# Kernel tuning notes

Measured on AMD Instinct MI355X. Metric: run time of the kernel, lower is better.

Reference implementation:

```python
import jax, jax.numpy as jnp
import numpy as np
from jax import lax

B, T, F_, CIN, COUT, NAUX = 32, 1000, 80, 1, 64, 128
KH, KW = 3, 3            # cnn_ker
CPAD = (1, 1)            # floor(k/2)
CSTR = (1, 1)
PK, PSTR = (2, 2), (2, 2)  # max-pool kernel/stride, pad 0


def setup_inputs() -> dict:
    key = jax.random.key(0)
    k1, k2, k3, k4, k5, k6, k7 = jax.random.split(key, 7)
    x = jax.random.normal(k1, (B, T, F_), dtype=jnp.float32)
    x_len = jax.random.randint(k2, (B,), 0, 1000).astype(jnp.int32)
    aux = jax.random.normal(k3, (B, NAUX), dtype=jnp.float32)
    # hypernetwork (filter/bias generator) params
    Wg = jax.random.normal(k4, (CIN * COUT * KH * KW, NAUX), dtype=jnp.float32) * 0.05
    bg = jax.random.normal(k5, (CIN * COUT * KH * KW,), dtype=jnp.float32) * 0.05
    Wb = jax.random.normal(k6, (COUT, NAUX), dtype=jnp.float32) * 0.05
    bb = jax.random.normal(k7, (COUT,), dtype=jnp.float32) * 0.05
    return {"x": x, "x_len": x_len, "aux": aux, "Wg": Wg, "bg": bg, "Wb": Wb, "bb": bb}


def _calclen(L, p, d, k, s):
    return (L + 2 * p - d * (k - 1) - 1) // s + 1


def reference(x, x_len, aux, Wg, bg, Wb, bb):
    # hypernetwork: per-sample conv filters [B, COUT, CIN, KH, KW] and biases [B, COUT]
    filt = (aux @ Wg.T + bg).reshape(B, COUT, CIN, KH, KW)
    bias = aux @ Wb.T + bb
    # per-sample conv as a single grouped conv: groups = B
    xg = x.reshape(1, B * CIN, T, F_)                 # x is [B, T, F] with CIN=1
    fg = filt.reshape(B * COUT, CIN, KH, KW)
    y = lax.conv_general_dilated(
        xg, fg, window_strides=CSTR,
        padding=[(CPAD[0], CPAD[0]), (CPAD[1], CPAD[1])],
        dimension_numbers=("NCHW", "OIHW", "NCHW"),
        feature_group_count=B)
    y = y.reshape(B, COUT, T, F_) + bias[:, :, None, None]
    # activ = relu
    y = jax.nn.relu(y)
    # max pool (2,2), stride (2,2), no pad
    y = lax.reduce_window(y, -jnp.inf, lax.max,
                          (1, 1, PK[0], PK[1]), (1, 1, PSTR[0], PSTR[1]), "VALID")
    # length propagation + time masking
    l1 = _calclen(x_len, CPAD[0], 1, KH, CSTR[0])
    l2 = _calclen(l1, 0, 1, PK[0], PSTR[0])
    t_out = y.shape[2]
    mask = jnp.arange(t_out)[None, :] >= l2[:, None]          # [B, T_out]
    y = jnp.where(mask[:, None, :, None], jnp.float32(0.0), y)
    return y, l2
```

## Files before the change

### kernel.cpp

```cpp
#include <hip/hip_runtime.h>
#include <hip/hip_fp16.h>
#include <stdint.h>

#define B_    32
#define T_    1000
#define F_    80
#define COUT_ 64
#define NAUX_ 128
#define TO_   500
#define FO_   40
#define PSTR_ 12
#define CL_   8

typedef float v4f __attribute__((ext_vector_type(4)));
typedef _Float16 h2v __attribute__((ext_vector_type(2)));
typedef __fp16 fp16x2 __attribute__((ext_vector_type(2)));

__global__ __launch_bounds__(256) void hyper_kernel(
    const float* __restrict__ aux,
    const float* __restrict__ Wg,
    const float* __restrict__ bg,
    const float* __restrict__ Wb,
    const float* __restrict__ bb,
    const int*   __restrict__ x_len,
    uint32_t* __restrict__ fw,
    float* __restrict__ l2_out)
{
    const int NFT = B_ * 576 * 16;
    const int NBT = B_ * 64 * 16;
    int t = blockIdx.x * blockDim.x + threadIdx.x;

    if (t < NFT) {
        int d = t >> 4, part = t & 15;
        int b = d / 576, idx = d % 576;
        const float* a = aux + b * NAUX_ + part * 8;
        const float* w = Wg + (size_t)idx * NAUX_ + part * 8;
        float4 a0 = *(const float4*)(a);
        float4 a1 = *(const float4*)(a + 4);
        float4 w0 = *(const float4*)(w);
        float4 w1 = *(const float4*)(w + 4);
        float s = a0.x * w0.x;
        s = fmaf(a0.y, w0.y, s);
        s = fmaf(a0.z, w0.z, s);
        s = fmaf(a0.w, w0.w, s);
        s = fmaf(a1.x, w1.x, s);
        s = fmaf(a1.y, w1.y, s);
        s = fmaf(a1.z, w1.z, s);
        s = fmaf(a1.w, w1.w, s);
        s += __shfl_xor(s, 1);
        s += __shfl_xor(s, 2);
        s += __shfl_xor(s, 4);
        s += __shfl_xor(s, 8);
        if (part == 0) {
            int c = idx / 9, k = idx % 9;
            uint32_t hu = (uint32_t)__half_as_ushort(__float2half_rn(s + bg[idx]));
            fw[(b * COUT_ + c) * PSTR_ + k] = hu | (hu << 16);
        }
    } else if (t < NFT + NBT) {
        int u = t - NFT;
        int d = u >> 4, part = u & 15;
        int b = d >> 6, c = d & 63;
        const float* a = aux + b * NAUX_ + part * 8;
        const float* w = Wb + (size_t)c * NAUX_ + part * 8;
        float4 a0 = *(const float4*)(a);
        float4 a1 = *(const float4*)(a + 4);
        float4 w0 = *(const float4*)(w);
        float4 w1 = *(const float4*)(w + 4);
        float s = a0.x * w0.x;
        s = fmaf(a0.y, w0.y, s);
        s = fmaf(a0.z, w0.z, s);
        s = fmaf(a0.w, w0.w, s);
        s = fmaf(a1.x, w1.x, s);
        s = fmaf(a1.y, w1.y, s);
        s = fmaf(a1.z, w1.z, s);
        s = fmaf(a1.w, w1.w, s);
        s += __shfl_xor(s, 1);
        s += __shfl_xor(s, 2);
        s += __shfl_xor(s, 4);
        s += __shfl_xor(s, 8);
        if (part == 0) fw[d * PSTR_ + 9] = __float_as_uint(s + bb[c]);
    } else if (t < NFT + NBT + B_) {
        int b = t - NFT - NBT;
        l2_out[b] = (float)(x_len[b] >> 1);
    }
}

__global__ __launch_bounds__(256) void conv_pool_kernel(
    const float*    __restrict__ x,
    const int*      __restrict__ x_len,
    const uint32_t* __restrict__ fw,
    float* __restrict__ out)
{
    const int bg  = blockIdx.y;
    const int b   = bg >> 3;
    const int bc0 = bg * CL_;

    int t = blockIdx.x * blockDim.x + threadIdx.x;
    if (t >= TO_ * 10) return;
    int f4 = t % 10;
    int to = t / 10;

    float* obase = out + ((size_t)bc0 * TO_ + to) * FO_ + 4 * f4;

    int l2 = x_len[b] >> 1;
    if (to >= l2) {
        v4f z = (v4f){0.f, 0.f, 0.f, 0.f};
        #pragma unroll
        for (int i = 0; i < CL_; ++i)
            __builtin_nontemporal_store(z, (v4f*)(obase + (size_t)i * (TO_ * FO_)));
        return;
    }

    const uint32_t* p = fw + (size_t)bc0 * PSTR_;
    uint32_t prm[CL_][10];
    #pragma unroll
    for (int i = 0; i < CL_; ++i)
        #pragma unroll
        for (int k = 0; k < 10; ++k)
            prm[i][k] = p[i * PSTR_ + k];

    float w[4][10];
    const float* xb = x + (size_t)b * (T_ * F_);
    const int cbase = 8 * f4;
    #pragma unroll
    for (int i = 0; i < 4; ++i) {
        int r = 2 * to - 1 + i;
        if (r < 0 || r >= T_) {
            #pragma unroll
            for (int j = 0; j < 10; ++j) w[i][j] = 0.f;
        } else {
            const float* rp = xb + r * F_ + cbase;
            w[i][0] = (f4 > 0) ? rp[-1] : 0.f;
            float4 m0 = *(const float4*)(rp);
            float4 m1 = *(const float4*)(rp + 4);
            w[i][1] = m0.x; w[i][2] = m0.y; w[i][3] = m0.z; w[i][4] = m0.w;
            w[i][5] = m1.x; w[i][6] = m1.y; w[i][7] = m1.z; w[i][8] = m1.w;
            w[i][9] = (f4 < 9) ? rp[8] : 0.f;
        }
    }

    __half2 wp[3][10];
    #pragma unroll
    for (int ii = 0; ii < 3; ++ii)
        #pragma unroll
        for (int c = 0; c < 10; ++c) {
            fp16x2 pk = __builtin_amdgcn_cvt_pkrtz(w[ii][c], w[ii + 1][c]);
            wp[ii][c] = *(__half2*)&pk;
        }

    #pragma unroll
    for (int i = 0; i < CL_; ++i) {
        __half2 flt[9];
        #pragma unroll
        for (int k = 0; k < 9; ++k)
            flt[k] = *(const __half2*)&prm[i][k];
        const float bias = __uint_as_float(prm[i][9]);

        float o[4];
        #pragma unroll
        for (int q = 0; q < 4; ++q) {
            __half2 acc0 = __halves2half2(__ushort_as_half((unsigned short)0),
                                          __ushort_as_half((unsigned short)0));
            __half2 acc1 = acc0;
            #pragma unroll
            for (int ii = 0; ii < 3; ++ii) {
                #pragma unroll
                for (int jj = 0; jj < 3; ++jj) {
                    const __half2 f = flt[ii * 3 + jj];
                    acc0 = __hfma2(f, wp[ii][2 * q + jj],     acc0);
                    acc1 = __hfma2(f, wp[ii][2 * q + 1 + jj], acc1);
                }
            }
            h2v m2 = __builtin_elementwise_max(*(h2v*)&acc0, *(h2v*)&acc1);
            float m = fmaxf((float)m2.x, (float)m2.y);
            o[q] = fmaxf(m + bias, 0.f);
        }
        v4f ov = (v4f){o[0], o[1], o[2], o[3]};
        __builtin_nontemporal_store(ov, (v4f*)(obase + (size_t)i * (TO_ * FO_)));
    }
}

extern "C" void kernel_launch(void* const* d_in, const int* in_sizes, int n_in,
                              void* d_out, int out_size, void* d_ws, size_t ws_size,
                              hipStream_t stream) {
    const float* x     = (const float*)d_in[0];
    const int*   x_len = (const int*)d_in[1];
    const float* aux   = (const float*)d_in[2];
    const float* Wg    = (const float*)d_in[3];
    const float* bg    = (const float*)d_in[4];
    const float* Wb    = (const float*)d_in[5];
    const float* bb    = (const float*)d_in[6];

    float*    out = (float*)d_out;
    uint32_t* fw  = (uint32_t*)d_ws;
    float* l2_out = out + (size_t)B_ * COUT_ * TO_ * FO_;

    {
        int total = B_ * 576 * 16 + B_ * 64 * 16 + B_;
        int blocks = (total + 255) / 256;
        hipLaunchKernelGGL(hyper_kernel, dim3(blocks), dim3(256), 0, stream,
                           aux, Wg, bg, Wb, bb, x_len, fw, l2_out);
    }
    {
        hipLaunchKernelGGL(conv_pool_kernel, dim3(20, 256), dim3(256), 0, stream,
                           x, x_len, fw, out);
    }
}
```

Before: 43.63 us.

## Pre-pack input row pairs to fp16x2 in workspace before conv-pool

The hyper kernel now also converts x into two packed fp16x2 buffers (odd-offset and even-offset row pairs). The conv-pool kernel then loads three packed rows instead of four fp32 rows and skips the per-thread conversion. This halves input read bytes in the conv kernel and removes redundant conversion across the 8 channel-group blocks that share a sample. In exchange it adds an extra write and read of about 10 MB of workspace, and it only runs when the workspace is large enough.

```diff
diff --git a/kernel.cpp b/kernel.cpp
--- a/kernel.cpp
+++ b/kernel.cpp
@@ -12,9 +12,24 @@
 #define PSTR_ 12
 #define CL_   8
 
+#define OFF_O 32768
+#define NO_U  (B_ * 501 * 80)
+#define OFF_E (OFF_O + NO_U)
+#define NE_U  (B_ * 500 * 80)
+
+#define NFT (B_ * 576 * 16)
+#define NBT (B_ * 64 * 16)
+#define NPP_O (B_ * 501 * 20)
+#define NPP_E (B_ * 500 * 20)
+
 typedef float v4f __attribute__((ext_vector_type(4)));
 typedef _Float16 h2v __attribute__((ext_vector_type(2)));
 typedef __fp16 fp16x2 __attribute__((ext_vector_type(2)));
+
+static __device__ __forceinline__ uint32_t pk2(float lo, float hi) {
+    fp16x2 pk = __builtin_amdgcn_cvt_pkrtz(lo, hi);
+    return *(uint32_t*)&pk;
+}
 
 __global__ __launch_bounds__(256) void hyper_kernel(
     const float* __restrict__ aux,
@@ -23,11 +38,10 @@
     const float* __restrict__ Wb,
     const float* __restrict__ bb,
     const int*   __restrict__ x_len,
-    uint32_t* __restrict__ fw,
+    const float* __restrict__ x,
+    uint32_t* __restrict__ ws,
     float* __restrict__ l2_out)
 {
-    const int NFT = B_ * 576 * 16;
-    const int NBT = B_ * 64 * 16;
     int t = blockIdx.x * blockDim.x + threadIdx.x;
 
     if (t < NFT) {
@@ -54,7 +68,7 @@
         if (part == 0) {
             int c = idx / 9, k = idx % 9;
             uint32_t hu = (uint32_t)__half_as_ushort(__float2half_rn(s + bg[idx]));
-            fw[(b * COUT_ + c) * PSTR_ + k] = hu | (hu << 16);
+            ws[(b * COUT_ + c) * PSTR_ + k] = hu | (hu << 16);
         }
     } else if (t < NFT + NBT) {
         int u = t - NFT;
@@ -78,17 +92,59 @@
         s += __shfl_xor(s, 2);
         s += __shfl_xor(s, 4);
         s += __shfl_xor(s, 8);
-        if (part == 0) fw[d * PSTR_ + 9] = __float_as_uint(s + bb[c]);
+        if (part == 0) ws[d * PSTR_ + 9] = __float_as_uint(s + bb[c]);
     } else if (t < NFT + NBT + B_) {
         int b = t - NFT - NBT;
         l2_out[b] = (float)(x_len[b] >> 1);
-    }
-}
-
+    } else if (t < NFT + NBT + B_ + NPP_O) {
+        int v  = t - (NFT + NBT + B_);
+        int b  = v / (501 * 20);
+        int r  = v % (501 * 20);
+        int to = r / 20;
+        int c  = (r % 20) * 4;
+        int rA = 2 * to - 1, rB = 2 * to;
+        float4 a = (rA >= 0) ? *(const float4*)(x + ((size_t)b * T_ + rA) * F_ + c)
+                             : make_float4(0.f, 0.f, 0.f, 0.f);
+        float4 d = (rB < T_) ? *(const float4*)(x + ((size_t)b * T_ + rB) * F_ + c)
+                             : make_float4(0.f, 0.f, 0.f, 0.f);
+        uint4 o;
+        o.x = pk2(a.x, d.x); o.y = pk2(a.y, d.y);
+        o.z = pk2(a.z, d.z); o.w = pk2(a.w, d.w);
+        *(uint4*)(ws + OFF_O + ((size_t)b * 501 + to) * 80 + c) = o;
+    } else if (t < NFT + NBT + B_ + NPP_O + NPP_E) {
+        int v  = t - (NFT + NBT + B_ + NPP_O);
+        int b  = v / (500 * 20);
+        int r  = v % (500 * 20);
+        int to = r / 20;
+        int c  = (r % 20) * 4;
+        const float* base = x + ((size_t)b * T_ + 2 * to) * F_ + c;
+        float4 a = *(const float4*)(base);
+        float4 d = *(const float4*)(base + F_);
+        uint4 o;
+        o.x = pk2(a.x, d.x); o.y = pk2(a.y, d.y);
+        o.z = pk2(a.z, d.z); o.w = pk2(a.w, d.w);
+        *(uint4*)(ws + OFF_E + ((size_t)b * 500 + to) * 80 + c) = o;
+    }
+}
+
+static __device__ __forceinline__ void load_prow(__half2* wp, const uint32_t* p, int f4) {
+    uint32_t u0 = (f4 > 0) ? p[-1] : 0u;
+    uint4 m0 = *(const uint4*)(p);
+    uint4 m1 = *(const uint4*)(p + 4);
+    uint32_t u9 = (f4 < 9) ? p[8] : 0u;
+    wp[0] = *(__half2*)&u0;
+    wp[1] = *(__half2*)&m0.x; wp[2] = *(__half2*)&m0.y;
+    wp[3] = *(__half2*)&m0.z; wp[4] = *(__half2*)&m0.w;
+    wp[5] = *(__half2*)&m1.x; wp[6] = *(__half2*)&m1.y;
+    wp[7] = *(__half2*)&m1.z; wp[8] = *(__half2*)&m1.w;
+    wp[9] = *(__half2*)&u9;
+}
+
+template<bool PRE>
 __global__ __launch_bounds__(256) void conv_pool_kernel(
     const float*    __restrict__ x,
     const int*      __restrict__ x_len,
-    const uint32_t* __restrict__ fw,
+    const uint32_t* __restrict__ ws,
     float* __restrict__ out)
 {
     const int bg  = blockIdx.y;
@@ -111,7 +167,7 @@
         return;
     }
 
-    const uint32_t* p = fw + (size_t)bc0 * PSTR_;
+    const uint32_t* p = ws + (size_t)bc0 * PSTR_;
     uint32_t prm[CL_][10];
     #pragma unroll
     for (int i = 0; i < CL_; ++i)
@@ -119,34 +175,42 @@
         for (int k = 0; k < 10; ++k)
             prm[i][k] = p[i * PSTR_ + k];
 
-    float w[4][10];
-    const float* xb = x + (size_t)b * (T_ * F_);
-    const int cbase = 8 * f4;
-    #pragma unroll
-    for (int i = 0; i < 4; ++i) {
-        int r = 2 * to - 1 + i;
-        if (r < 0 || r >= T_) {
+    __half2 wp[3][10];
+    const int cb = 8 * f4;
+
+    if (PRE) {
+        const uint32_t* Ob = ws + OFF_O + ((size_t)b * 501 + to) * 80 + cb;
+        const uint32_t* Eb = ws + OFF_E + ((size_t)b * 500 + to) * 80 + cb;
+        load_prow(wp[0], Ob, f4);
+        load_prow(wp[1], Eb, f4);
+        load_prow(wp[2], Ob + 80, f4);
+    } else {
+        float w[4][10];
+        const float* xb = x + (size_t)b * (T_ * F_);
+        #pragma unroll
+        for (int i = 0; i < 4; ++i) {
+            int r = 2 * to - 1 + i;
+            if (r < 0 || r >= T_) {
+                #pragma unroll
+                for (int j = 0; j < 10; ++j) w[i][j] = 0.f;
+            } else {
+                const float* rp = xb + r * F_ + cb;
+                w[i][0] = (f4 > 0) ? rp[-1] : 0.f;
+                float4 m0 = *(const float4*)(rp);
+                float4 m1 = *(const float4*)(rp + 4);
+                w[i][1] = m0.x; w[i][2] = m0.y; w[i][3] = m0.z; w[i][4] = m0.w;
+                w[i][5] = m1.x; w[i][6] = m1.y; w[i][7] = m1.z; w[i][8] = m1.w;
+                w[i][9] = (f4 < 9) ? rp[8] : 0.f;
+            }
+        }
+        #pragma unroll
+        for (int ii = 0; ii < 3; ++ii)
             #pragma unroll
-            for (int j = 0; j < 10; ++j) w[i][j] = 0.f;
-        } else {
-            const float* rp = xb + r * F_ + cbase;
-            w[i][0] = (f4 > 0) ? rp[-1] : 0.f;
-            float4 m0 = *(const float4*)(rp);
-            float4 m1 = *(const float4*)(rp + 4);
-            w[i][1] = m0.x; w[i][2] = m0.y; w[i][3] = m0.z; w[i][4] = m0.w;
-            w[i][5] = m1.x; w[i][6] = m1.y; w[i][7] = m1.z; w[i][8] = m1.w;
-            w[i][9] = (f4 < 9) ? rp[8] : 0.f;
-        }
-    }
-
-    __half2 wp[3][10];
-    #pragma unroll
-    for (int ii = 0; ii < 3; ++ii)
-        #pragma unroll
-        for (int c = 0; c < 10; ++c) {
-            fp16x2 pk = __builtin_amdgcn_cvt_pkrtz(w[ii][c], w[ii + 1][c]);
-            wp[ii][c] = *(__half2*)&pk;
-        }
+            for (int c = 0; c < 10; ++c) {
+                uint32_t u = pk2(w[ii][c], w[ii + 1][c]);
+                wp[ii][c] = *(__half2*)&u;
+            }
+    }
 
     #pragma unroll
     for (int i = 0; i < CL_; ++i) {
@@ -192,17 +256,23 @@
     const float* bb    = (const float*)d_in[6];
 
     float*    out = (float*)d_out;
-    uint32_t* fw  = (uint32_t*)d_ws;
+    uint32_t* ws  = (uint32_t*)d_ws;
     float* l2_out = out + (size_t)B_ * COUT_ * TO_ * FO_;
 
+    const size_t need = (size_t)(OFF_E + NE_U) * 4;
+    const bool pre = (ws_size >= need);
+
     {
-        int total = B_ * 576 * 16 + B_ * 64 * 16 + B_;
+        int total = NFT + NBT + B_ + (pre ? (NPP_O + NPP_E) : 0);
         int blocks = (total + 255) / 256;
         hipLaunchKernelGGL(hyper_kernel, dim3(blocks), dim3(256), 0, stream,
-                           aux, Wg, bg, Wb, bb, x_len, fw, l2_out);
-    }
-    {
-        hipLaunchKernelGGL(conv_pool_kernel, dim3(20, 256), dim3(256), 0, stream,
-                           x, x_len, fw, out);
-    }
-}
+                           aux, Wg, bg, Wb, bb, x_len, x, ws, l2_out);
+    }
+    if (pre) {
+        hipLaunchKernelGGL((conv_pool_kernel<true>), dim3(20, 256), dim3(256), 0, stream,
+                           x, x_len, ws, out);
+    } else {
+        hipLaunchKernelGGL((conv_pool_kernel<false>), dim3(20, 256), dim3(256), 0, stream,
+                           x, x_len, ws, out);
+    }
+}
```

Result: slower. 45.04 us (+3.2%).
